# Optimization experiments

Hardware: AMD Instinct MI355X
Metric: run time of the kernel (lower is better)

## Reference

```python
import jax, jax.numpy as jnp
import numpy as np

T, B, F, H, N = 256, 256, 128, 1024, 2


def setup_inputs() -> dict:
    key = jax.random.key(0)
    ks = jax.random.split(key, 12)
    s_in = 1.0 / np.sqrt(H)  # PyTorch LSTM/Linear init scale ~ U(-1/sqrt(H), 1/sqrt(H))
    u = lambda k, shape: jax.random.uniform(k, shape, jnp.float32, -s_in, s_in)
    inp = {
        "x": jax.random.normal(ks[0], (T, B, F), jnp.float32),
        "W_ih0": u(ks[1], (4 * H, F)),
        "W_hh0": u(ks[2], (4 * H, H)),
        "b_ih0": u(ks[3], (4 * H,)),
        "b_hh0": u(ks[4], (4 * H,)),
        "W_ih1": u(ks[5], (4 * H, H)),
        "W_hh1": u(ks[6], (4 * H, H)),
        "b_ih1": u(ks[7], (4 * H,)),
        "b_hh1": u(ks[8], (4 * H,)),
        "W_lin": u(ks[9], (F, H)),
        "b_lin": u(ks[10], (F,)),
        "bs": B,
    }
    return inp


def _lstm_layer(x, W_ih, W_hh, b_ih, b_hh):
    # x: (T, B, in), returns out (T, B, H), (h_T, c_T) each (B, H)
    # Precompute input projections for all timesteps in one big GEMM.
    xW = jnp.einsum('tbf,gf->tbg', x, W_ih) + b_ih + b_hh  # (T, B, 4H)
    h0 = jnp.zeros((x.shape[1], W_hh.shape[1]), x.dtype)

    def step(carry, xw_t):
        h, c = carry
        gates = xw_t + h @ W_hh.T  # (B, 4H); PyTorch gate order i, f, g, o
        i, f, g, o = jnp.split(gates, 4, axis=-1)
        c = jax.nn.sigmoid(f) * c + jax.nn.sigmoid(i) * jnp.tanh(g)
        h = jax.nn.sigmoid(o) * jnp.tanh(c)
        return (h, c), h

    (h_T, c_T), out = jax.lax.scan(step, (h0, h0), xW)
    return out, h_T, c_T


def reference(x, W_ih0, W_hh0, b_ih0, b_hh0, W_ih1, W_hh1, b_ih1, b_hh1, W_lin, b_lin, bs):
    # Stacked 2-layer LSTM with zero initial state (self.h is None on fresh call).
    out0, h0_T, c0_T = _lstm_layer(x, W_ih0, W_hh0, b_ih0, b_hh0)
    out1, h1_T, c1_T = _lstm_layer(out0, W_ih1, W_hh1, b_ih1, b_hh1)
    # Original: y = linear(out[0]) -> first timestep of top layer output.
    y = out1[0] @ W_lin.T + b_lin  # (B, F)
    h_n = jnp.stack([h0_T, h1_T])  # (N, B, H)
    c_n = jnp.stack([c0_T, c1_T])  # (N, B, H)
    return y, h_n, c_n
```

## Files before the change

kernel.cpp:

```cpp
#include <hip/hip_runtime.h>
#include <stdint.h>


typedef __bf16 bf16x8 __attribute__((ext_vector_type(8)));
typedef float  f32x4  __attribute__((ext_vector_type(4)));
typedef unsigned short ushort8v __attribute__((ext_vector_type(8)));
typedef unsigned short ushort4v __attribute__((ext_vector_type(4)));
typedef unsigned short ushort2v __attribute__((ext_vector_type(2)));
typedef unsigned int   uint4v   __attribute__((ext_vector_type(4)));
typedef __attribute__((address_space(1))) unsigned int as1_u32;
typedef __attribute__((address_space(3))) unsigned int as3_u32;

#define T_STEPS 256
#define BATCH   256
#define HDIM    1024
#define GDIM    4096
#define FDIM    128
#define AS_STRIDE 2080

static __device__ __forceinline__ float bf2f(unsigned short u) {
  union { unsigned int i; float f; } v; v.i = ((unsigned int)u) << 16; return v.f;
}
static __device__ __forceinline__ unsigned short f2bf(float f) {
  return __builtin_bit_cast(unsigned short, (__bf16)f);
}
static __device__ __forceinline__ float sigm(float x) { return 1.f / (1.f + __expf(-x)); }
static __device__ __forceinline__ float tanh_f(float x) { return 2.f / (1.f + __expf(-2.f * x)) - 1.f; }

static __device__ __forceinline__ void vl1_inv() {
  asm volatile("buffer_inv" ::: "memory");
}

__global__ void conv_bf16(const float* __restrict__ s, unsigned short* __restrict__ d, int n) {
  int i = blockIdx.x * 256 + threadIdx.x;
  if (i < n) d[i] = f2bf(s[i]);
}

__global__ void diag_kernel(float* out, int n, float v) {
  int i = blockIdx.x * 256 + threadIdx.x;
  if (i < n) out[i] = v;
}

__device__ __forceinline__ void grp_arrive(unsigned int* gbar, bool fast) {
  __syncthreads();
  if (threadIdx.x == 0) {
    if (!fast) __builtin_amdgcn_fence(__ATOMIC_RELEASE, "agent");
    unsigned int my = __hip_atomic_fetch_add(&gbar[0], 1u, __ATOMIC_RELAXED, __HIP_MEMORY_SCOPE_AGENT);
    if ((my & 31u) == 31u)
      __hip_atomic_fetch_add(&gbar[32], 1u, __ATOMIC_RELAXED, __HIP_MEMORY_SCOPE_AGENT);
  }
}

__device__ __forceinline__ void grp_wait(unsigned int* gbar, unsigned int target, bool fast) {
  for (unsigned int it = 0; it < (1u << 14); ++it) {
    unsigned int g = __hip_atomic_load(&gbar[32], __ATOMIC_RELAXED, __HIP_MEMORY_SCOPE_AGENT);
    if ((int)(g - target) >= 0) break;
    __builtin_amdgcn_s_sleep(1);
  }
  if (!fast) __builtin_amdgcn_fence(__ATOMIC_ACQUIRE, "agent");
  else vl1_inv();
}

__device__ __forceinline__ void grp_barrier(unsigned int* gbar, unsigned int target, bool fast) {
  grp_arrive(gbar, fast);
  grp_wait(gbar, target, fast);
  __syncthreads();
}

__global__ __launch_bounds__(256) void gemm_bt_xw(
    const unsigned short* __restrict__ A,
    const unsigned short* __restrict__ B,
    unsigned short* __restrict__ xw,
    int K)
{
  const int tid = threadIdx.x, lane = tid & 63, w = tid >> 6;
  const int m0 = blockIdx.x * 128;
  const int n0 = blockIdx.y * 128;
  __shared__ unsigned short As[128 * 64];
  __shared__ unsigned short Bs[128 * 64];
  const int mrow0 = (w & 1) * 64, ncol0 = (w >> 1) * 64;
  const int quad = lane >> 4;

  f32x4 acc[4][4];
  #pragma unroll
  for (int i = 0; i < 4; ++i)
    #pragma unroll
    for (int j = 0; j < 4; ++j) acc[i][j] = f32x4{0.f, 0.f, 0.f, 0.f};

  const int kiter = K >> 6;
  for (int ki = 0; ki < kiter; ++ki) {
    const int k0 = ki * 64;
    __syncthreads();
    #pragma unroll
    for (int i = 0; i < 4; ++i) {
      int obase = (w * 4 + i) * 1024;
      int o = obase + lane * 16;
      int row = o >> 7; int kb = o & 127;
      const char* ga = (const char*)A + ((size_t)(m0 + row) * K + k0) * 2 + kb;
      const char* gb = (const char*)B + ((size_t)(n0 + row) * K + k0) * 2 + kb;
      __builtin_amdgcn_global_load_lds((const as1_u32*)ga, (as3_u32*)((char*)As + obase), 16, 0, 0);
      __builtin_amdgcn_global_load_lds((const as1_u32*)gb, (as3_u32*)((char*)Bs + obase), 16, 0, 0);
    }
    __syncthreads();
    #pragma unroll
    for (int kk = 0; kk < 2; ++kk) {
      bf16x8 af[4], bfr[4];
      #pragma unroll
      for (int mt = 0; mt < 4; ++mt)
        af[mt] = *(const bf16x8*)(As + (mrow0 + mt * 16 + (lane & 15)) * 64 + kk * 32 + quad * 8);
      #pragma unroll
      for (int nt = 0; nt < 4; ++nt)
        bfr[nt] = *(const bf16x8*)(Bs + (ncol0 + nt * 16 + (lane & 15)) * 64 + kk * 32 + quad * 8);
      #pragma unroll
      for (int mt = 0; mt < 4; ++mt)
        #pragma unroll
        for (int nt = 0; nt < 4; ++nt)
          acc[mt][nt] = __builtin_amdgcn_mfma_f32_16x16x32_bf16(af[mt], bfr[nt], acc[mt][nt], 0, 0, 0);
    }
  }
  #pragma unroll
  for (int mt = 0; mt < 4; ++mt) {
    int m = m0 + mrow0 + mt * 16 + quad * 4;
    int tl = m >> 8, b = m & 255;
    #pragma unroll
    for (int nt = 0; nt < 4; ++nt) {
      int col = n0 + ncol0 + nt * 16 + (lane & 15);
      ushort4v v;
      v.x = f2bf(acc[mt][nt][0]); v.y = f2bf(acc[mt][nt][1]);
      v.z = f2bf(acc[mt][nt][2]); v.w = f2bf(acc[mt][nt][3]);
      *(ushort4v*)(xw + ((size_t)tl * GDIM + col) * BATCH + b) = v;
    }
  }
}

__device__ __forceinline__ bool probe_fast(unsigned int* probe, unsigned int* gbar,
                                           unsigned int salt, unsigned int target,
                                           unsigned int* flagLds) {
  const int wg = blockIdx.x, mi = wg & 7;
  if (threadIdx.x == 0) probe[wg * 32] = salt ^ (unsigned int)wg;
  grp_barrier(gbar, target, true);
  if (threadIdx.x == 0) {
    unsigned int bad = 0;
    for (int k = 0; k < 32; ++k) {
      int member = mi + 8 * k;
      unsigned int v = probe[member * 32];
      if (v != (salt ^ (unsigned int)member)) bad = 1;
    }
    *flagLds = bad;
  }
  __syncthreads();
  return (*flagLds == 0);
}

__global__ __launch_bounds__(512, 2) void lstm_layer0_kernel(
    const unsigned short* __restrict__ xbf,
    const float* __restrict__ Wih,
    const float* __restrict__ Whh,
    const float* __restrict__ bih,
    const float* __restrict__ bhh,
    unsigned short* __restrict__ slab,
    float* __restrict__ cstate,
    int t0, int ch_len, unsigned int gen_base,
    float* __restrict__ dout_h,
    float* __restrict__ dout_c,
    unsigned int* __restrict__ bar,
    unsigned int* __restrict__ probe)
{
  const int tid = threadIdx.x, lane = tid & 63, wv = tid >> 6;
  const int quad = lane >> 4, l15 = lane & 15;
  const int g = wv & 3, kh = wv >> 2;
  const int wg = blockIdx.x;
  const int mi = wg & 7, ni = wg >> 3;
  const int r0 = mi * 32, hc0 = ni * 32;
  unsigned int* gbar = bar + mi * 64;

  __shared__ unsigned short As[32 * (AS_STRIDE / 2)];
  __shared__ float gbuf[8][32][36];
  __shared__ unsigned int flagLds;

  bf16x8 whh[2][16];
  #pragma unroll
  for (int nt = 0; nt < 2; ++nt) {
    const float* wrow = Whh + (size_t)(g * HDIM + hc0 + nt * 16 + l15) * HDIM + kh * 512 + quad * 8;
    #pragma unroll
    for (int kk = 0; kk < 16; ++kk) {
      f32x4 f0 = *(const f32x4*)(wrow + kk * 32);
      f32x4 f1 = *(const f32x4*)(wrow + kk * 32 + 4);
      bf16x8 r;
      r[0] = (__bf16)f0[0]; r[1] = (__bf16)f0[1]; r[2] = (__bf16)f0[2]; r[3] = (__bf16)f0[3];
      r[4] = (__bf16)f1[0]; r[5] = (__bf16)f1[1]; r[6] = (__bf16)f1[2]; r[7] = (__bf16)f1[3];
      whh[nt][kk] = r;
    }
  }
  bf16x8 wih[2][2];
  #pragma unroll
  for (int nt = 0; nt < 2; ++nt) {
    const float* wrow = Wih + (size_t)(g * HDIM + hc0 + nt * 16 + l15) * FDIM + kh * 64 + quad * 8;
    #pragma unroll
    for (int kk = 0; kk < 2; ++kk) {
      f32x4 f0 = *(const f32x4*)(wrow + kk * 32);
      f32x4 f1 = *(const f32x4*)(wrow + kk * 32 + 4);
      bf16x8 r;
      r[0] = (__bf16)f0[0]; r[1] = (__bf16)f0[1]; r[2] = (__bf16)f0[2]; r[3] = (__bf16)f0[3];
      r[4] = (__bf16)f1[0]; r[5] = (__bf16)f1[1]; r[6] = (__bf16)f1[2]; r[7] = (__bf16)f1[3];
      wih[nt][kk] = r;
    }
  }

  const int hcl = tid & 31, rg2 = tid >> 5;
  float bias[4];
  #pragma unroll
  for (int b4 = 0; b4 < 4; ++b4)
    bias[b4] = bih[b4 * HDIM + hc0 + hcl] + bhh[b4 * HDIM + hc0 + hcl];

  float c[2];
  #pragma unroll
  for (int r = 0; r < 2; ++r)
    c[r] = (t0 == 0) ? 0.f : cstate[(size_t)(r0 + rg2 * 2 + r) * HDIM + hc0 + hcl];

  unsigned int salt = 0x9E3779B9u ^ (gen_base * 2654435761u);
  bool fast = probe_fast(probe, gbar, salt, gen_base + 1u, &flagLds);

  const int tend = t0 + ch_len;

  f32x4 acc[2][2];
  #pragma unroll
  for (int mt = 0; mt < 2; ++mt)
    #pragma unroll
    for (int nt = 0; nt < 2; ++nt) acc[mt][nt] = f32x4{0.f, 0.f, 0.f, 0.f};
  #pragma unroll
  for (int j = 0; j < 2; ++j) {
    bf16x8 af[2];
    #pragma unroll
    for (int mt = 0; mt < 2; ++mt)
      af[mt] = *(const bf16x8*)(xbf + (size_t)(t0 * BATCH + r0 + mt * 16 + l15) * FDIM + kh * 64 + j * 32 + quad * 8);
    #pragma unroll
    for (int mt = 0; mt < 2; ++mt)
      #pragma unroll
      for (int nt = 0; nt < 2; ++nt)
        acc[mt][nt] = __builtin_amdgcn_mfma_f32_16x16x32_bf16(af[mt], wih[nt][j], acc[mt][nt], 0, 0, 0);
  }

  #pragma unroll 1
  for (int t = t0; t < tend; ++t) {
    if (t > 0) {
      const unsigned short* Aprev = slab + (size_t)(t - t0) * (BATCH * HDIM);
      #pragma unroll
      for (int p = 0; p < 8; ++p) {
        int idx = p * 8 + wv;
        int row = idx >> 1, half = idx & 1;
        const char* gsrc = (const char*)(Aprev + (size_t)(r0 + row) * HDIM + half * 512) + lane * 16;
        char* ldst = (char*)As + row * AS_STRIDE + half * 1024;
        __builtin_amdgcn_global_load_lds((const as1_u32*)gsrc, (as3_u32*)ldst, 16, 0, 0);
      }
      __syncthreads();
      #pragma unroll
      for (int j = 0; j < 16; ++j) {
        bf16x8 af[2];
        #pragma unroll
        for (int mt = 0; mt < 2; ++mt)
          af[mt] = *(const bf16x8*)((const char*)As + (mt * 16 + l15) * AS_STRIDE + (kh * 16 + j) * 64 + quad * 16);
        #pragma unroll
        for (int mt = 0; mt < 2; ++mt)
          #pragma unroll
          for (int nt = 0; nt < 2; ++nt)
            acc[mt][nt] = __builtin_amdgcn_mfma_f32_16x16x32_bf16(af[mt], whh[nt][j], acc[mt][nt], 0, 0, 0);
      }
    }

    __syncthreads();
    #pragma unroll
    for (int mt = 0; mt < 2; ++mt)
      #pragma unroll
      for (int nt = 0; nt < 2; ++nt) {
        int hl = nt * 16 + l15;
        int rq = mt * 16 + quad * 4;
        *(f32x4*)&gbuf[wv][hl][rq] = acc[mt][nt];
      }
    __syncthreads();

    unsigned short* hdst = slab + (size_t)(t - t0 + 1) * (BATCH * HDIM);
    unsigned short* hdst0 = slab;
    #pragma unroll
    for (int r = 0; r < 2; ++r) {
      int row = rg2 * 2 + r;
      float gi = gbuf[0][hcl][row] + gbuf[4][hcl][row] + bias[0];
      float gf = gbuf[1][hcl][row] + gbuf[5][hcl][row] + bias[1];
      float gg = gbuf[2][hcl][row] + gbuf[6][hcl][row] + bias[2];
      float go = gbuf[3][hcl][row] + gbuf[7][hcl][row] + bias[3];
      float iv = sigm(gi), fv = sigm(gf), gv = tanh_f(gg), ov = sigm(go);
      float cn = fv * c[r] + iv * gv;
      c[r] = cn;
      float hv = ov * tanh_f(cn);
      int gidx = (r0 + row) * HDIM + hc0 + hcl;
      unsigned short hb = f2bf(hv);
      hdst[gidx] = hb;
      if (t == tend - 1) { hdst0[gidx] = hb; cstate[gidx] = cn; }
      if (t == T_STEPS - 1) { dout_h[gidx] = hv; dout_c[gidx] = cn; }
    }

    if (t != tend - 1) {
      grp_arrive(gbar, fast);
      #pragma unroll
      for (int mt = 0; mt < 2; ++mt)
        #pragma unroll
        for (int nt = 0; nt < 2; ++nt) acc[mt][nt] = f32x4{0.f, 0.f, 0.f, 0.f};
      #pragma unroll
      for (int j = 0; j < 2; ++j) {
        bf16x8 af[2];
        #pragma unroll
        for (int mt = 0; mt < 2; ++mt)
          af[mt] = *(const bf16x8*)(xbf + (size_t)((t + 1) * BATCH + r0 + mt * 16 + l15) * FDIM + kh * 64 + j * 32 + quad * 8);
        #pragma unroll
        for (int mt = 0; mt < 2; ++mt)
          #pragma unroll
          for (int nt = 0; nt < 2; ++nt)
            acc[mt][nt] = __builtin_amdgcn_mfma_f32_16x16x32_bf16(af[mt], wih[nt][j], acc[mt][nt], 0, 0, 0);
      }
      grp_wait(gbar, gen_base + 2u + (unsigned int)(t - t0), fast);
    }
  }
}

__global__ __launch_bounds__(512, 2) void lstm_layer1_kernel(
    const unsigned short* __restrict__ xw,
    const float* __restrict__ Whh,
    const float* __restrict__ bih,
    const float* __restrict__ bhh,
    unsigned short* __restrict__ hpp,
    float* __restrict__ cstate,
    int t0, int ch_len, unsigned int gen_base,
    unsigned short* __restrict__ h1t0,
    float* __restrict__ dout_h,
    float* __restrict__ dout_c,
    unsigned int* __restrict__ bar,
    unsigned int* __restrict__ probe)
{
  const int tid = threadIdx.x, lane = tid & 63, wv = tid >> 6;
  const int quad = lane >> 4, l15 = lane & 15;
  const int g = wv & 3, kh = wv >> 2;
  const int wg = blockIdx.x;
  const int mi = wg & 7, ni = wg >> 3;
  const int r0 = mi * 32, hc0 = ni * 32;
  unsigned int* gbar = bar + mi * 64;

  __shared__ unsigned short As[32 * (AS_STRIDE / 2)];
  __shared__ float gbuf[8][32][36];
  __shared__ unsigned int flagLds;

  bf16x8 whh[2][16];
  #pragma unroll
  for (int nt = 0; nt < 2; ++nt) {
    const float* wrow = Whh + (size_t)(g * HDIM + hc0 + nt * 16 + l15) * HDIM + kh * 512 + quad * 8;
    #pragma unroll
    for (int kk = 0; kk < 16; ++kk) {
      f32x4 f0 = *(const f32x4*)(wrow + kk * 32);
      f32x4 f1 = *(const f32x4*)(wrow + kk * 32 + 4);
      bf16x8 r;
      r[0] = (__bf16)f0[0]; r[1] = (__bf16)f0[1]; r[2] = (__bf16)f0[2]; r[3] = (__bf16)f0[3];
      r[4] = (__bf16)f1[0]; r[5] = (__bf16)f1[1]; r[6] = (__bf16)f1[2]; r[7] = (__bf16)f1[3];
      whh[nt][kk] = r;
    }
  }

  const int hcl = tid & 31, rg2 = tid >> 5;
  float bias[4];
  #pragma unroll
  for (int b4 = 0; b4 < 4; ++b4)
    bias[b4] = bih[b4 * HDIM + hc0 + hcl] + bhh[b4 * HDIM + hc0 + hcl];

  float c[2];
  #pragma unroll
  for (int r = 0; r < 2; ++r)
    c[r] = (t0 == 0) ? 0.f : cstate[(size_t)(r0 + rg2 * 2 + r) * HDIM + hc0 + hcl];

  unsigned int salt = 0xB5297A4Du ^ (gen_base * 2654435761u);
  bool fast = probe_fast(probe, gbar, salt, gen_base + 1u, &flagLds);

  const int tend = t0 + ch_len;

  float xwv[4][2];
  #pragma unroll
  for (int g4 = 0; g4 < 4; ++g4) {
    const unsigned short* xp =
        xw + ((size_t)0 * GDIM + g4 * HDIM + hc0 + hcl) * BATCH + r0 + rg2 * 2;
    ushort2v u = *(const ushort2v*)xp;
    xwv[g4][0] = bf2f(u.x); xwv[g4][1] = bf2f(u.y);
  }

  #pragma unroll 1
  for (int t = t0; t < tend; ++t) {
    f32x4 acc[2][2];
    #pragma unroll
    for (int mt = 0; mt < 2; ++mt)
      #pragma unroll
      for (int nt = 0; nt < 2; ++nt) acc[mt][nt] = f32x4{0.f, 0.f, 0.f, 0.f};

    if (t > 0) {
      const unsigned short* Aprev = hpp + (size_t)((t - 1) & 1) * (BATCH * HDIM);
      #pragma unroll
      for (int p = 0; p < 8; ++p) {
        int idx = p * 8 + wv;
        int row = idx >> 1, half = idx & 1;
        const char* gsrc = (const char*)(Aprev + (size_t)(r0 + row) * HDIM + half * 512) + lane * 16;
        char* ldst = (char*)As + row * AS_STRIDE + half * 1024;
        __builtin_amdgcn_global_load_lds((const as1_u32*)gsrc, (as3_u32*)ldst, 16, 0, 0);
      }
      __syncthreads();
      #pragma unroll
      for (int j = 0; j < 16; ++j) {
        bf16x8 af[2];
        #pragma unroll
        for (int mt = 0; mt < 2; ++mt)
          af[mt] = *(const bf16x8*)((const char*)As + (mt * 16 + l15) * AS_STRIDE + (kh * 16 + j) * 64 + quad * 16);
        #pragma unroll
        for (int mt = 0; mt < 2; ++mt)
          #pragma unroll
          for (int nt = 0; nt < 2; ++nt)
            acc[mt][nt] = __builtin_amdgcn_mfma_f32_16x16x32_bf16(af[mt], whh[nt][j], acc[mt][nt], 0, 0, 0);
      }
    }

    __syncthreads();
    #pragma unroll
    for (int mt = 0; mt < 2; ++mt)
      #pragma unroll
      for (int nt = 0; nt < 2; ++nt) {
        int hl = nt * 16 + l15;
        int rq = mt * 16 + quad * 4;
        *(f32x4*)&gbuf[wv][hl][rq] = acc[mt][nt];
      }
    __syncthreads();

    unsigned short* hdst = hpp + (size_t)(t & 1) * (BATCH * HDIM);
    #pragma unroll
    for (int r = 0; r < 2; ++r) {
      int row = rg2 * 2 + r;
      float gi = gbuf[0][hcl][row] + gbuf[4][hcl][row] + xwv[0][r] + bias[0];
      float gf = gbuf[1][hcl][row] + gbuf[5][hcl][row] + xwv[1][r] + bias[1];
      float gg = gbuf[2][hcl][row] + gbuf[6][hcl][row] + xwv[2][r] + bias[2];
      float go = gbuf[3][hcl][row] + gbuf[7][hcl][row] + xwv[3][r] + bias[3];
      float iv = sigm(gi), fv = sigm(gf), gv = tanh_f(gg), ov = sigm(go);
      float cn = fv * c[r] + iv * gv;
      c[r] = cn;
      float hv = ov * tanh_f(cn);
      int gidx = (r0 + row) * HDIM + hc0 + hcl;
      hdst[gidx] = f2bf(hv);
      if (h1t0 != nullptr && t == 0) h1t0[gidx] = f2bf(hv);
      if (t == tend - 1) cstate[gidx] = cn;
      if (t == T_STEPS - 1) { dout_h[gidx] = hv; dout_c[gidx] = cn; }
    }

    if (t != tend - 1) {
      grp_arrive(gbar, fast);
      #pragma unroll
      for (int g4 = 0; g4 < 4; ++g4) {
        const unsigned short* xp =
            xw + ((size_t)(t + 1 - t0) * GDIM + g4 * HDIM + hc0 + hcl) * BATCH + r0 + rg2 * 2;
        ushort2v u = *(const ushort2v*)xp;
        xwv[g4][0] = bf2f(u.x); xwv[g4][1] = bf2f(u.y);
      }
      grp_wait(gbar, gen_base + 2u + (unsigned int)(t - t0), fast);
    }
  }
}

__global__ void y_kernel(const unsigned short* __restrict__ h1t0,
                         const unsigned short* __restrict__ wlin,
                         const float* __restrict__ blin,
                         float* __restrict__ y)
{
  int b = blockIdx.x;
  int f = threadIdx.x;
  const ushort8v* hp = (const ushort8v*)(h1t0 + (size_t)b * HDIM);
  const ushort8v* wp = (const ushort8v*)(wlin + (size_t)f * HDIM);
  float acc = 0.f;
  for (int i = 0; i < HDIM / 8; ++i) {
    ushort8v hv = hp[i], wvv = wp[i];
    #pragma unroll
    for (int j = 0; j < 8; ++j) acc += bf2f(hv[j]) * bf2f(wvv[j]);
  }
  y[b * FDIM + f] = acc + blin[f];
}

extern "C" void kernel_launch(void* const* d_in, const int* in_sizes, int n_in,
                              void* d_out, int out_size, void* d_ws, size_t ws_size,
                              hipStream_t stream) {
  (void)in_sizes; (void)n_in; (void)out_size;
  const float* x    = (const float*)d_in[0];
  const float* Wih0 = (const float*)d_in[1];
  const float* Whh0 = (const float*)d_in[2];
  const float* bih0 = (const float*)d_in[3];
  const float* bhh0 = (const float*)d_in[4];
  const float* Wih1 = (const float*)d_in[5];
  const float* Whh1 = (const float*)d_in[6];
  const float* bih1 = (const float*)d_in[7];
  const float* bhh1 = (const float*)d_in[8];
  const float* Wlin = (const float*)d_in[9];
  const float* blin = (const float*)d_in[10];
  float* out = (float*)d_out;

  const size_t SZ_BAR   = 4096;
  const size_t SZ_PROBE = 32768;
  const size_t SZ_XBF   = (size_t)T_STEPS * BATCH * FDIM * 2;
  const size_t SZ_WIH1  = (size_t)GDIM * HDIM * 2;
  const size_t SZ_WLIN  = (size_t)FDIM * HDIM * 2;
  const size_t SZ_HPP   = (size_t)2 * BATCH * HDIM * 2;
  const size_t SZ_H1T0  = (size_t)BATCH * HDIM * 2;
  const size_t SZ_CST   = (size_t)BATCH * HDIM * 4;
  const size_t SLOT     = (size_t)BATCH * HDIM * 2;
  const size_t fixed = SZ_BAR + SZ_PROBE + SZ_XBF + SZ_WIH1 + SZ_WLIN + SZ_HPP + SZ_H1T0 + 2 * SZ_CST;

  int CH = 0;
  const int cands[5] = {64, 32, 16, 8, 4};
  for (int i = 0; i < 5; ++i) {
    int c = cands[i];
    size_t need = fixed + (size_t)(c + 1) * SLOT + (size_t)c * GDIM * BATCH * 2;
    if (need <= ws_size) { CH = c; break; }
  }
  if (CH == 0) {
    float v = 1.0e6f + (float)(ws_size >> 20);
    diag_kernel<<<(32768 + 255) / 256, 256, 0, stream>>>(out, 32768, v);
    return;
  }

  char* ws = (char*)d_ws;
  size_t o = 0;
  unsigned int*   bar   = (unsigned int*)(ws + o);    o += SZ_BAR;
  unsigned int*   probe = (unsigned int*)(ws + o);    o += SZ_PROBE;
  unsigned short* xbf   = (unsigned short*)(ws + o);  o += SZ_XBF;
  unsigned short* wih1b = (unsigned short*)(ws + o);  o += SZ_WIH1;
  unsigned short* wlinb = (unsigned short*)(ws + o);  o += SZ_WLIN;
  unsigned short* h1pp  = (unsigned short*)(ws + o);  o += SZ_HPP;
  unsigned short* h1t0  = (unsigned short*)(ws + o);  o += SZ_H1T0;
  float*          c0st  = (float*)(ws + o);           o += SZ_CST;
  float*          c1st  = (float*)(ws + o);           o += SZ_CST;
  unsigned short* slab  = (unsigned short*)(ws + o);  o += (size_t)(CH + 1) * SLOT;
  unsigned short* xw1   = (unsigned short*)(ws + o);  o += (size_t)CH * GDIM * BATCH * 2;

  hipMemsetAsync(bar, 0, SZ_BAR, stream);

  conv_bf16<<<(T_STEPS * BATCH * FDIM + 255) / 256, 256, 0, stream>>>(x, xbf, T_STEPS * BATCH * FDIM);
  conv_bf16<<<(GDIM * HDIM + 255) / 256, 256, 0, stream>>>(Wih1, wih1b, GDIM * HDIM);
  conv_bf16<<<(FDIM * HDIM + 255) / 256, 256, 0, stream>>>(Wlin, wlinb, FDIM * HDIM);

  float* hn0 = out + 32768;
  float* hn1 = out + 32768 + 262144;
  float* cn0 = out + 32768 + 524288;
  float* cn1 = out + 32768 + 524288 + 262144;

  unsigned int gen_base = 0;
  for (int ch = 0; ch < T_STEPS / CH; ++ch) {
    int t0 = ch * CH;
    lstm_layer0_kernel<<<256, 512, 0, stream>>>(
        xbf, Wih0, Whh0, bih0, bhh0, slab, c0st, t0, CH, gen_base, hn0, cn0, bar, probe);
    gen_base += (unsigned int)CH;
    gemm_bt_xw<<<dim3(CH * 2, 32), 256, 0, stream>>>(
        slab + BATCH * HDIM, wih1b, xw1, HDIM);
    lstm_layer1_kernel<<<256, 512, 0, stream>>>(
        xw1, Whh1, bih1, bhh1, h1pp, c1st, t0, CH, gen_base, h1t0, hn1, cn1, bar, probe);
    gen_base += (unsigned int)CH;
  }

  y_kernel<<<256, 128, 0, stream>>>(h1t0, wlinb, blin, out);
}
```

Measured before the change: 3.631 ms.

## Split recurrent K dimension four ways with 1024-thread LSTM blocks

```diff
diff --git a/kernel.cpp b/kernel.cpp
--- a/kernel.cpp
+++ b/kernel.cpp
@@ -6,7 +6,6 @@
 typedef float  f32x4  __attribute__((ext_vector_type(4)));
 typedef unsigned short ushort8v __attribute__((ext_vector_type(8)));
 typedef unsigned short ushort4v __attribute__((ext_vector_type(4)));
-typedef unsigned short ushort2v __attribute__((ext_vector_type(2)));
 typedef unsigned int   uint4v   __attribute__((ext_vector_type(4)));
 typedef __attribute__((address_space(1))) unsigned int as1_u32;
 typedef __attribute__((address_space(3))) unsigned int as3_u32;
@@ -16,7 +15,7 @@
 #define HDIM    1024
 #define GDIM    4096
 #define FDIM    128
-#define AS_STRIDE 2080
+#define AS_STRIDE 2096
 
 static __device__ __forceinline__ float bf2f(unsigned short u) {
   union { unsigned int i; float f; } v; v.i = ((unsigned int)u) << 16; return v.f;
@@ -51,20 +50,22 @@
   }
 }
 
-__device__ __forceinline__ void grp_wait(unsigned int* gbar, unsigned int target, bool fast) {
-  for (unsigned int it = 0; it < (1u << 14); ++it) {
-    unsigned int g = __hip_atomic_load(&gbar[32], __ATOMIC_RELAXED, __HIP_MEMORY_SCOPE_AGENT);
-    if ((int)(g - target) >= 0) break;
-    __builtin_amdgcn_s_sleep(1);
-  }
-  if (!fast) __builtin_amdgcn_fence(__ATOMIC_ACQUIRE, "agent");
-  else vl1_inv();
-}
-
-__device__ __forceinline__ void grp_barrier(unsigned int* gbar, unsigned int target, bool fast) {
+__device__ __forceinline__ void grp_wait_w0(unsigned int* gbar, unsigned int target, bool fast, int wv) {
+  if (wv == 0) {
+    for (unsigned int it = 0; it < (1u << 14); ++it) {
+      unsigned int g = __hip_atomic_load(&gbar[32], __ATOMIC_RELAXED, __HIP_MEMORY_SCOPE_AGENT);
+      if ((int)(g - target) >= 0) break;
+      __builtin_amdgcn_s_sleep(1);
+    }
+    if (!fast) __builtin_amdgcn_fence(__ATOMIC_ACQUIRE, "agent");
+  }
+  __syncthreads();
+  if (fast) vl1_inv();
+}
+
+__device__ __forceinline__ void grp_barrier(unsigned int* gbar, unsigned int target, bool fast, int wv) {
   grp_arrive(gbar, fast);
-  grp_wait(gbar, target, fast);
-  __syncthreads();
+  grp_wait_w0(gbar, target, fast, wv);
 }
 
 __global__ __launch_bounds__(256) void gemm_bt_xw(
@@ -135,10 +136,10 @@
 
 __device__ __forceinline__ bool probe_fast(unsigned int* probe, unsigned int* gbar,
                                            unsigned int salt, unsigned int target,
-                                           unsigned int* flagLds) {
+                                           unsigned int* flagLds, int wv) {
   const int wg = blockIdx.x, mi = wg & 7;
   if (threadIdx.x == 0) probe[wg * 32] = salt ^ (unsigned int)wg;
-  grp_barrier(gbar, target, true);
+  grp_barrier(gbar, target, true, wv);
   if (threadIdx.x == 0) {
     unsigned int bad = 0;
     for (int k = 0; k < 32; ++k) {
@@ -152,13 +153,14 @@
   return (*flagLds == 0);
 }
 
-__global__ __launch_bounds__(512, 2) void lstm_layer0_kernel(
+__global__ __launch_bounds__(1024, 4) void lstm_layer0_kernel(
     const unsigned short* __restrict__ xbf,
     const float* __restrict__ Wih,
     const float* __restrict__ Whh,
     const float* __restrict__ bih,
     const float* __restrict__ bhh,
     unsigned short* __restrict__ slab,
+    unsigned short* __restrict__ hx,
     float* __restrict__ cstate,
     int t0, int ch_len, unsigned int gen_base,
     float* __restrict__ dout_h,
@@ -168,22 +170,22 @@
 {
   const int tid = threadIdx.x, lane = tid & 63, wv = tid >> 6;
   const int quad = lane >> 4, l15 = lane & 15;
-  const int g = wv & 3, kh = wv >> 2;
+  const int g = wv & 3, kq = wv >> 2;
   const int wg = blockIdx.x;
   const int mi = wg & 7, ni = wg >> 3;
   const int r0 = mi * 32, hc0 = ni * 32;
   unsigned int* gbar = bar + mi * 64;
 
   __shared__ unsigned short As[32 * (AS_STRIDE / 2)];
-  __shared__ float gbuf[8][32][36];
+  __shared__ float gbuf[16][32][33];
   __shared__ unsigned int flagLds;
 
-  bf16x8 whh[2][16];
+  bf16x8 whh[2][8];
   #pragma unroll
   for (int nt = 0; nt < 2; ++nt) {
-    const float* wrow = Whh + (size_t)(g * HDIM + hc0 + nt * 16 + l15) * HDIM + kh * 512 + quad * 8;
-    #pragma unroll
-    for (int kk = 0; kk < 16; ++kk) {
+    const float* wrow = Whh + (size_t)(g * HDIM + hc0 + nt * 16 + l15) * HDIM + kq * 256 + quad * 8;
+    #pragma unroll
+    for (int kk = 0; kk < 8; ++kk) {
       f32x4 f0 = *(const f32x4*)(wrow + kk * 32);
       f32x4 f1 = *(const f32x4*)(wrow + kk * 32 + 4);
       bf16x8 r;
@@ -192,34 +194,28 @@
       whh[nt][kk] = r;
     }
   }
-  bf16x8 wih[2][2];
+  bf16x8 wih[2];
   #pragma unroll
   for (int nt = 0; nt < 2; ++nt) {
-    const float* wrow = Wih + (size_t)(g * HDIM + hc0 + nt * 16 + l15) * FDIM + kh * 64 + quad * 8;
-    #pragma unroll
-    for (int kk = 0; kk < 2; ++kk) {
-      f32x4 f0 = *(const f32x4*)(wrow + kk * 32);
-      f32x4 f1 = *(const f32x4*)(wrow + kk * 32 + 4);
-      bf16x8 r;
-      r[0] = (__bf16)f0[0]; r[1] = (__bf16)f0[1]; r[2] = (__bf16)f0[2]; r[3] = (__bf16)f0[3];
-      r[4] = (__bf16)f1[0]; r[5] = (__bf16)f1[1]; r[6] = (__bf16)f1[2]; r[7] = (__bf16)f1[3];
-      wih[nt][kk] = r;
-    }
-  }
-
-  const int hcl = tid & 31, rg2 = tid >> 5;
+    const float* wrow = Wih + (size_t)(g * HDIM + hc0 + nt * 16 + l15) * FDIM + kq * 32 + quad * 8;
+    f32x4 f0 = *(const f32x4*)(wrow);
+    f32x4 f1 = *(const f32x4*)(wrow + 4);
+    bf16x8 r;
+    r[0] = (__bf16)f0[0]; r[1] = (__bf16)f0[1]; r[2] = (__bf16)f0[2]; r[3] = (__bf16)f0[3];
+    r[4] = (__bf16)f1[0]; r[5] = (__bf16)f1[1]; r[6] = (__bf16)f1[2]; r[7] = (__bf16)f1[3];
+    wih[nt] = r;
+  }
+
+  const int hcl = tid & 31, row = tid >> 5;
   float bias[4];
   #pragma unroll
   for (int b4 = 0; b4 < 4; ++b4)
     bias[b4] = bih[b4 * HDIM + hc0 + hcl] + bhh[b4 * HDIM + hc0 + hcl];
 
-  float c[2];
-  #pragma unroll
-  for (int r = 0; r < 2; ++r)
-    c[r] = (t0 == 0) ? 0.f : cstate[(size_t)(r0 + rg2 * 2 + r) * HDIM + hc0 + hcl];
+  float c1 = (t0 == 0) ? 0.f : cstate[(size_t)(r0 + row) * HDIM + hc0 + hcl];
 
   unsigned int salt = 0x9E3779B9u ^ (gen_base * 2654435761u);
-  bool fast = probe_fast(probe, gbar, salt, gen_base + 1u, &flagLds);
+  bool fast = probe_fast(probe, gbar, salt, gen_base + 1u, &flagLds, wv);
 
   const int tend = t0 + ch_len;
 
@@ -228,38 +224,37 @@
   for (int mt = 0; mt < 2; ++mt)
     #pragma unroll
     for (int nt = 0; nt < 2; ++nt) acc[mt][nt] = f32x4{0.f, 0.f, 0.f, 0.f};
-  #pragma unroll
-  for (int j = 0; j < 2; ++j) {
+  {
     bf16x8 af[2];
     #pragma unroll
     for (int mt = 0; mt < 2; ++mt)
-      af[mt] = *(const bf16x8*)(xbf + (size_t)(t0 * BATCH + r0 + mt * 16 + l15) * FDIM + kh * 64 + j * 32 + quad * 8);
+      af[mt] = *(const bf16x8*)(xbf + (size_t)(t0 * BATCH + r0 + mt * 16 + l15) * FDIM + kq * 32 + quad * 8);
     #pragma unroll
     for (int mt = 0; mt < 2; ++mt)
       #pragma unroll
       for (int nt = 0; nt < 2; ++nt)
-        acc[mt][nt] = __builtin_amdgcn_mfma_f32_16x16x32_bf16(af[mt], wih[nt][j], acc[mt][nt], 0, 0, 0);
+        acc[mt][nt] = __builtin_amdgcn_mfma_f32_16x16x32_bf16(af[mt], wih[nt], acc[mt][nt], 0, 0, 0);
   }
 
   #pragma unroll 1
   for (int t = t0; t < tend; ++t) {
     if (t > 0) {
-      const unsigned short* Aprev = slab + (size_t)(t - t0) * (BATCH * HDIM);
-      #pragma unroll
-      for (int p = 0; p < 8; ++p) {
-        int idx = p * 8 + wv;
-        int row = idx >> 1, half = idx & 1;
-        const char* gsrc = (const char*)(Aprev + (size_t)(r0 + row) * HDIM + half * 512) + lane * 16;
-        char* ldst = (char*)As + row * AS_STRIDE + half * 1024;
+      const unsigned short* Aprev = hx + (size_t)((t - 1) & 1) * (BATCH * HDIM);
+      #pragma unroll
+      for (int p = 0; p < 4; ++p) {
+        int idx = p * 16 + wv;
+        int arow = idx >> 1, half = idx & 1;
+        const char* gsrc = (const char*)(Aprev + (size_t)(r0 + arow) * HDIM + half * 512) + lane * 16;
+        char* ldst = (char*)As + arow * AS_STRIDE + half * 1024;
         __builtin_amdgcn_global_load_lds((const as1_u32*)gsrc, (as3_u32*)ldst, 16, 0, 0);
       }
       __syncthreads();
       #pragma unroll
-      for (int j = 0; j < 16; ++j) {
+      for (int j = 0; j < 8; ++j) {
         bf16x8 af[2];
         #pragma unroll
         for (int mt = 0; mt < 2; ++mt)
-          af[mt] = *(const bf16x8*)((const char*)As + (mt * 16 + l15) * AS_STRIDE + (kh * 16 + j) * 64 + quad * 16);
+          af[mt] = *(const bf16x8*)((const char*)As + (mt * 16 + l15) * AS_STRIDE + kq * 512 + j * 64 + quad * 16);
         #pragma unroll
         for (int mt = 0; mt < 2; ++mt)
           #pragma unroll
@@ -275,27 +270,28 @@
       for (int nt = 0; nt < 2; ++nt) {
         int hl = nt * 16 + l15;
         int rq = mt * 16 + quad * 4;
-        *(f32x4*)&gbuf[wv][hl][rq] = acc[mt][nt];
+        #pragma unroll
+        for (int i = 0; i < 4; ++i)
+          gbuf[wv][hl][rq + i] = acc[mt][nt][i];
       }
     __syncthreads();
 
     unsigned short* hdst = slab + (size_t)(t - t0 + 1) * (BATCH * HDIM);
-    unsigned short* hdst0 = slab;
-    #pragma unroll
-    for (int r = 0; r < 2; ++r) {
-      int row = rg2 * 2 + r;
-      float gi = gbuf[0][hcl][row] + gbuf[4][hcl][row] + bias[0];
-      float gf = gbuf[1][hcl][row] + gbuf[5][hcl][row] + bias[1];
-      float gg = gbuf[2][hcl][row] + gbuf[6][hcl][row] + bias[2];
-      float go = gbuf[3][hcl][row] + gbuf[7][hcl][row] + bias[3];
+    unsigned short* hxd  = hx + (size_t)(t & 1) * (BATCH * HDIM);
+    {
+      float gi = gbuf[0][hcl][row] + gbuf[4][hcl][row] + gbuf[8][hcl][row]  + gbuf[12][hcl][row] + bias[0];
+      float gf = gbuf[1][hcl][row] + gbuf[5][hcl][row] + gbuf[9][hcl][row]  + gbuf[13][hcl][row] + bias[1];
+      float gg = gbuf[2][hcl][row] + gbuf[6][hcl][row] + gbuf[10][hcl][row] + gbuf[14][hcl][row] + bias[2];
+      float go = gbuf[3][hcl][row] + gbuf[7][hcl][row] + gbuf[11][hcl][row] + gbuf[15][hcl][row] + bias[3];
       float iv = sigm(gi), fv = sigm(gf), gv = tanh_f(gg), ov = sigm(go);
-      float cn = fv * c[r] + iv * gv;
-      c[r] = cn;
+      float cn = fv * c1 + iv * gv;
+      c1 = cn;
       float hv = ov * tanh_f(cn);
       int gidx = (r0 + row) * HDIM + hc0 + hcl;
       unsigned short hb = f2bf(hv);
+      hxd[gidx] = hb;
       hdst[gidx] = hb;
-      if (t == tend - 1) { hdst0[gidx] = hb; cstate[gidx] = cn; }
+      if (t == tend - 1) cstate[gidx] = cn;
       if (t == T_STEPS - 1) { dout_h[gidx] = hv; dout_c[gidx] = cn; }
     }
 
@@ -305,24 +301,23 @@
       for (int mt = 0; mt < 2; ++mt)
         #pragma unroll
         for (int nt = 0; nt < 2; ++nt) acc[mt][nt] = f32x4{0.f, 0.f, 0.f, 0.f};
-      #pragma unroll
-      for (int j = 0; j < 2; ++j) {
+      {
         bf16x8 af[2];
         #pragma unroll
         for (int mt = 0; mt < 2; ++mt)
-          af[mt] = *(const bf16x8*)(xbf + (size_t)((t + 1) * BATCH + r0 + mt * 16 + l15) * FDIM + kh * 64 + j * 32 + quad * 8);
+          af[mt] = *(const bf16x8*)(xbf + (size_t)((t + 1) * BATCH + r0 + mt * 16 + l15) * FDIM + kq * 32 + quad * 8);
         #pragma unroll
         for (int mt = 0; mt < 2; ++mt)
           #pragma unroll
           for (int nt = 0; nt < 2; ++nt)
-            acc[mt][nt] = __builtin_amdgcn_mfma_f32_16x16x32_bf16(af[mt], wih[nt][j], acc[mt][nt], 0, 0, 0);
-      }
-      grp_wait(gbar, gen_base + 2u + (unsigned int)(t - t0), fast);
-    }
-  }
-}
-
-__global__ __launch_bounds__(512, 2) void lstm_layer1_kernel(
+            acc[mt][nt] = __builtin_amdgcn_mfma_f32_16x16x32_bf16(af[mt], wih[nt], acc[mt][nt], 0, 0, 0);
+      }
+      grp_wait_w0(gbar, gen_base + 2u + (unsigned int)(t - t0), fast, wv);
+    }
+  }
+}
+
+__global__ __launch_bounds__(1024, 4) void lstm_layer1_kernel(
     const unsigned short* __restrict__ xw,
     const float* __restrict__ Whh,
     const float* __restrict__ bih,
@@ -338,22 +333,22 @@
 {
   const int tid = threadIdx.x, lane = tid & 63, wv = tid >> 6;
   const int quad = lane >> 4, l15 = lane & 15;
-  const int g = wv & 3, kh = wv >> 2;
+  const int g = wv & 3, kq = wv >> 2;
   const int wg = blockIdx.x;
   const int mi = wg & 7, ni = wg >> 3;
   const int r0 = mi * 32, hc0 = ni * 32;
   unsigned int* gbar = bar + mi * 64;
 
   __shared__ unsigned short As[32 * (AS_STRIDE / 2)];
-  __shared__ float gbuf[8][32][36];
+  __shared__ float gbuf[16][32][33];
   __shared__ unsigned int flagLds;
 
-  bf16x8 whh[2][16];
+  bf16x8 whh[2][8];
   #pragma unroll
   for (int nt = 0; nt < 2; ++nt) {
-    const float* wrow = Whh + (size_t)(g * HDIM + hc0 + nt * 16 + l15) * HDIM + kh * 512 + quad * 8;
-    #pragma unroll
-    for (int kk = 0; kk < 16; ++kk) {
+    const float* wrow = Whh + (size_t)(g * HDIM + hc0 + nt * 16 + l15) * HDIM + kq * 256 + quad * 8;
+    #pragma unroll
+    for (int kk = 0; kk < 8; ++kk) {
       f32x4 f0 = *(const f32x4*)(wrow + kk * 32);
       f32x4 f1 = *(const f32x4*)(wrow + kk * 32 + 4);
       bf16x8 r;
@@ -363,29 +358,25 @@
     }
   }
 
-  const int hcl = tid & 31, rg2 = tid >> 5;
+  const int hcl = tid & 31, row = tid >> 5;
   float bias[4];
   #pragma unroll
   for (int b4 = 0; b4 < 4; ++b4)
     bias[b4] = bih[b4 * HDIM + hc0 + hcl] + bhh[b4 * HDIM + hc0 + hcl];
 
-  float c[2];
-  #pragma unroll
-  for (int r = 0; r < 2; ++r)
-    c[r] = (t0 == 0) ? 0.f : cstate[(size_t)(r0 + rg2 * 2 + r) * HDIM + hc0 + hcl];
+  float c1 = (t0 == 0) ? 0.f : cstate[(size_t)(r0 + row) * HDIM + hc0 + hcl];
 
   unsigned int salt = 0xB5297A4Du ^ (gen_base * 2654435761u);
-  bool fast = probe_fast(probe, gbar, salt, gen_base + 1u, &flagLds);
+  bool fast = probe_fast(probe, gbar, salt, gen_base + 1u, &flagLds, wv);
 
   const int tend = t0 + ch_len;
 
-  float xwv[4][2];
+  float xwv[4];
   #pragma unroll
   for (int g4 = 0; g4 < 4; ++g4) {
     const unsigned short* xp =
-        xw + ((size_t)0 * GDIM + g4 * HDIM + hc0 + hcl) * BATCH + r0 + rg2 * 2;
-    ushort2v u = *(const ushort2v*)xp;
-    xwv[g4][0] = bf2f(u.x); xwv[g4][1] = bf2f(u.y);
+        xw + ((size_t)0 * GDIM + g4 * HDIM + hc0 + hcl) * BATCH + r0 + row;
+    xwv[g4] = bf2f(*xp);
   }
 
   #pragma unroll 1
@@ -399,20 +390,20 @@
     if (t > 0) {
       const unsigned short* Aprev = hpp + (size_t)((t - 1) & 1) * (BATCH * HDIM);
       #pragma unroll
-      for (int p = 0; p < 8; ++p) {
-        int idx = p * 8 + wv;
-        int row = idx >> 1, half = idx & 1;
-        const char* gsrc = (const char*)(Aprev + (size_t)(r0 + row) * HDIM + half * 512) + lane * 16;
-        char* ldst = (char*)As + row * AS_STRIDE + half * 1024;
+      for (int p = 0; p < 4; ++p) {
+        int idx = p * 16 + wv;
+        int arow = idx >> 1, half = idx & 1;
+        const char* gsrc = (const char*)(Aprev + (size_t)(r0 + arow) * HDIM + half * 512) + lane * 16;
+        char* ldst = (char*)As + arow * AS_STRIDE + half * 1024;
         __builtin_amdgcn_global_load_lds((const as1_u32*)gsrc, (as3_u32*)ldst, 16, 0, 0);
       }
       __syncthreads();
       #pragma unroll
-      for (int j = 0; j < 16; ++j) {
+      for (int j = 0; j < 8; ++j) {
         bf16x8 af[2];
         #pragma unroll
         for (int mt = 0; mt < 2; ++mt)
-          af[mt] = *(const bf16x8*)((const char*)As + (mt * 16 + l15) * AS_STRIDE + (kh * 16 + j) * 64 + quad * 16);
+          af[mt] = *(const bf16x8*)((const char*)As + (mt * 16 + l15) * AS_STRIDE + kq * 512 + j * 64 + quad * 16);
         #pragma unroll
         for (int mt = 0; mt < 2; ++mt)
           #pragma unroll
@@ -428,21 +419,21 @@
       for (int nt = 0; nt < 2; ++nt) {
         int hl = nt * 16 + l15;
         int rq = mt * 16 + quad * 4;
-        *(f32x4*)&gbuf[wv][hl][rq] = acc[mt][nt];
+        #pragma unroll
+        for (int i = 0; i < 4; ++i)
+          gbuf[wv][hl][rq + i] = acc[mt][nt][i];
       }
     __syncthreads();
 
     unsigned short* hdst = hpp + (size_t)(t & 1) * (BATCH * HDIM);
-    #pragma unroll
-    for (int r = 0; r < 2; ++r) {
-      int row = rg2 * 2 + r;
-      float gi = gbuf[0][hcl][row] + gbuf[4][hcl][row] + xwv[0][r] + bias[0];
-      float gf = gbuf[1][hcl][row] + gbuf[5][hcl][row] + xwv[1][r] + bias[1];
-      float gg = gbuf[2][hcl][row] + gbuf[6][hcl][row] + xwv[2][r] + bias[2];
-      float go = gbuf[3][hcl][row] + gbuf[7][hcl][row] + xwv[3][r] + bias[3];
+    {
+      float gi = gbuf[0][hcl][row] + gbuf[4][hcl][row] + gbuf[8][hcl][row]  + gbuf[12][hcl][row] + xwv[0] + bias[0];
+      float gf = gbuf[1][hcl][row] + gbuf[5][hcl][row] + gbuf[9][hcl][row]  + gbuf[13][hcl][row] + xwv[1] + bias[1];
+      float gg = gbuf[2][hcl][row] + gbuf[6][hcl][row] + gbuf[10][hcl][row] + gbuf[14][hcl][row] + xwv[2] + bias[2];
+      float go = gbuf[3][hcl][row] + gbuf[7][hcl][row] + gbuf[11][hcl][row] + gbuf[15][hcl][row] + xwv[3] + bias[3];
       float iv = sigm(gi), fv = sigm(gf), gv = tanh_f(gg), ov = sigm(go);
-      float cn = fv * c[r] + iv * gv;
-      c[r] = cn;
+      float cn = fv * c1 + iv * gv;
+      c1 = cn;
       float hv = ov * tanh_f(cn);
       int gidx = (r0 + row) * HDIM + hc0 + hcl;
       hdst[gidx] = f2bf(hv);
@@ -456,11 +447,10 @@
       #pragma unroll
       for (int g4 = 0; g4 < 4; ++g4) {
         const unsigned short* xp =
-            xw + ((size_t)(t + 1 - t0) * GDIM + g4 * HDIM + hc0 + hcl) * BATCH + r0 + rg2 * 2;
-        ushort2v u = *(const ushort2v*)xp;
-        xwv[g4][0] = bf2f(u.x); xwv[g4][1] = bf2f(u.y);
-      }
-      grp_wait(gbar, gen_base + 2u + (unsigned int)(t - t0), fast);
+            xw + ((size_t)(t + 1 - t0) * GDIM + g4 * HDIM + hc0 + hcl) * BATCH + r0 + row;
+        xwv[g4] = bf2f(*xp);
+      }
+      grp_wait_w0(gbar, gen_base + 2u + (unsigned int)(t - t0), fast, wv);
     }
   }
 }
@@ -506,10 +496,11 @@
   const size_t SZ_WIH1  = (size_t)GDIM * HDIM * 2;
   const size_t SZ_WLIN  = (size_t)FDIM * HDIM * 2;
   const size_t SZ_HPP   = (size_t)2 * BATCH * HDIM * 2;
+  const size_t SZ_HX    = (size_t)2 * BATCH * HDIM * 2;
   const size_t SZ_H1T0  = (size_t)BATCH * HDIM * 2;
   const size_t SZ_CST   = (size_t)BATCH * HDIM * 4;
   const size_t SLOT     = (size_t)BATCH * HDIM * 2;
-  const size_t fixed = SZ_BAR + SZ_PROBE + SZ_XBF + SZ_WIH1 + SZ_WLIN + SZ_HPP + SZ_H1T0 + 2 * SZ_CST;
+  const size_t fixed = SZ_BAR + SZ_PROBE + SZ_XBF + SZ_WIH1 + SZ_WLIN + SZ_HPP + SZ_HX + SZ_H1T0 + 2 * SZ_CST;
 
   int CH = 0;
   const int cands[5] = {64, 32, 16, 8, 4};
@@ -532,6 +523,7 @@
   unsigned short* wih1b = (unsigned short*)(ws + o);  o += SZ_WIH1;
   unsigned short* wlinb = (unsigned short*)(ws + o);  o += SZ_WLIN;
   unsigned short* h1pp  = (unsigned short*)(ws + o);  o += SZ_HPP;
+  unsigned short* hx0   = (unsigned short*)(ws + o);  o += SZ_HX;
   unsigned short* h1t0  = (unsigned short*)(ws + o);  o += SZ_H1T0;
   float*          c0st  = (float*)(ws + o);           o += SZ_CST;
   float*          c1st  = (float*)(ws + o);           o += SZ_CST;
@@ -552,12 +544,12 @@
   unsigned int gen_base = 0;
   for (int ch = 0; ch < T_STEPS / CH; ++ch) {
     int t0 = ch * CH;
-    lstm_layer0_kernel<<<256, 512, 0, stream>>>(
-        xbf, Wih0, Whh0, bih0, bhh0, slab, c0st, t0, CH, gen_base, hn0, cn0, bar, probe);
+    lstm_layer0_kernel<<<256, 1024, 0, stream>>>(
+        xbf, Wih0, Whh0, bih0, bhh0, slab, hx0, c0st, t0, CH, gen_base, hn0, cn0, bar, probe);
     gen_base += (unsigned int)CH;
     gemm_bt_xw<<<dim3(CH * 2, 32), 256, 0, stream>>>(
         slab + BATCH * HDIM, wih1b, xw1, HDIM);
-    lstm_layer1_kernel<<<256, 512, 0, stream>>>(
+    lstm_layer1_kernel<<<256, 1024, 0, stream>>>(
         xw1, Whh1, bih1, bhh1, h1pp, c1st, t0, CH, gen_base, h1t0, hn1, cn1, bar, probe);
     gen_base += (unsigned int)CH;
   }
```

After: 3.956 ms. 9.0% more time.

## Replace counter barrier with per-block stamp polling and prefetch h into LDS

Applied to the files above, without the earlier changes.

```diff
diff --git a/kernel.cpp b/kernel.cpp
--- a/kernel.cpp
+++ b/kernel.cpp
@@ -41,30 +41,30 @@
   if (i < n) out[i] = v;
 }
 
-__device__ __forceinline__ void grp_arrive(unsigned int* gbar, bool fast) {
-  __syncthreads();
-  if (threadIdx.x == 0) {
-    if (!fast) __builtin_amdgcn_fence(__ATOMIC_RELEASE, "agent");
-    unsigned int my = __hip_atomic_fetch_add(&gbar[0], 1u, __ATOMIC_RELAXED, __HIP_MEMORY_SCOPE_AGENT);
-    if ((my & 31u) == 31u)
-      __hip_atomic_fetch_add(&gbar[32], 1u, __ATOMIC_RELAXED, __HIP_MEMORY_SCOPE_AGENT);
-  }
-}
-
-__device__ __forceinline__ void grp_wait(unsigned int* gbar, unsigned int target, bool fast) {
-  for (unsigned int it = 0; it < (1u << 14); ++it) {
-    unsigned int g = __hip_atomic_load(&gbar[32], __ATOMIC_RELAXED, __HIP_MEMORY_SCOPE_AGENT);
-    if ((int)(g - target) >= 0) break;
-    __builtin_amdgcn_s_sleep(1);
-  }
-  if (!fast) __builtin_amdgcn_fence(__ATOMIC_ACQUIRE, "agent");
-  else vl1_inv();
-}
-
-__device__ __forceinline__ void grp_barrier(unsigned int* gbar, unsigned int target, bool fast) {
-  grp_arrive(gbar, fast);
-  grp_wait(gbar, target, fast);
-  __syncthreads();
+__device__ __forceinline__ void post_stamp(unsigned int* st, unsigned int gen, bool fast) {
+  if (!fast) __builtin_amdgcn_fence(__ATOMIC_RELEASE, "agent");
+  __hip_atomic_store(st, gen, __ATOMIC_RELAXED, __HIP_MEMORY_SCOPE_AGENT);
+}
+
+__device__ __forceinline__ void poll_all(unsigned int* stamps, unsigned int target) {
+  unsigned int* p = stamps + (threadIdx.x & 31) * 32;
+  for (unsigned int it = 0; it < (1u << 15); ++it) {
+    unsigned int gv = __hip_atomic_load(p, __ATOMIC_RELAXED, __HIP_MEMORY_SCOPE_AGENT);
+    if (__all((int)(gv - target) >= 0)) return;
+    if (it > 16) __builtin_amdgcn_s_sleep(1);
+  }
+}
+
+__device__ __forceinline__ void stage64(const unsigned short* __restrict__ hsrc,
+                                        char* AsB, int r0, int wv, int lane) {
+  #pragma unroll
+  for (int p = 0; p < 8; ++p) {
+    int idx = p * 8 + wv;
+    int row = idx >> 1, half = idx & 1;
+    const char* gsrc = (const char*)(hsrc + (size_t)(r0 + row) * HDIM + half * 512) + lane * 16;
+    char* ldst = AsB + row * AS_STRIDE + half * 1024;
+    __builtin_amdgcn_global_load_lds((const as1_u32*)gsrc, (as3_u32*)ldst, 16, 0, 0);
+  }
 }
 
 __global__ __launch_bounds__(256) void gemm_bt_xw(
@@ -133,17 +133,22 @@
   }
 }
 
-__device__ __forceinline__ bool probe_fast(unsigned int* probe, unsigned int* gbar,
-                                           unsigned int salt, unsigned int target,
-                                           unsigned int* flagLds) {
-  const int wg = blockIdx.x, mi = wg & 7;
-  if (threadIdx.x == 0) probe[wg * 32] = salt ^ (unsigned int)wg;
-  grp_barrier(gbar, target, true);
-  if (threadIdx.x == 0) {
+__device__ __forceinline__ bool probe_chk(unsigned int* probeBuf, unsigned int* stamps,
+                                          unsigned int salt, unsigned int target,
+                                          unsigned int* flagLds) {
+  const int wg = blockIdx.x, mi = wg & 7, ni = wg >> 3;
+  const int tid = threadIdx.x;
+  if (tid == 0) probeBuf[wg * 32] = salt ^ (unsigned int)wg;
+  __syncthreads();
+  if (tid == 0)
+    __hip_atomic_store(stamps + ni * 32, target, __ATOMIC_RELAXED, __HIP_MEMORY_SCOPE_AGENT);
+  poll_all(stamps, target);
+  vl1_inv();
+  if (tid == 0) {
     unsigned int bad = 0;
     for (int k = 0; k < 32; ++k) {
       int member = mi + 8 * k;
-      unsigned int v = probe[member * 32];
+      unsigned int v = probeBuf[member * 32];
       if (v != (salt ^ (unsigned int)member)) bad = 1;
     }
     *flagLds = bad;
@@ -159,6 +164,7 @@
     const float* __restrict__ bih,
     const float* __restrict__ bhh,
     unsigned short* __restrict__ slab,
+    unsigned short* __restrict__ hx,
     float* __restrict__ cstate,
     int t0, int ch_len, unsigned int gen_base,
     float* __restrict__ dout_h,
@@ -172,7 +178,7 @@
   const int wg = blockIdx.x;
   const int mi = wg & 7, ni = wg >> 3;
   const int r0 = mi * 32, hc0 = ni * 32;
-  unsigned int* gbar = bar + mi * 64;
+  unsigned int* stamps = bar + mi * 1024;
 
   __shared__ unsigned short As[32 * (AS_STRIDE / 2)];
   __shared__ float gbuf[8][32][36];
@@ -219,9 +225,12 @@
     c[r] = (t0 == 0) ? 0.f : cstate[(size_t)(r0 + rg2 * 2 + r) * HDIM + hc0 + hcl];
 
   unsigned int salt = 0x9E3779B9u ^ (gen_base * 2654435761u);
-  bool fast = probe_fast(probe, gbar, salt, gen_base + 1u, &flagLds);
+  bool fast = probe_chk(probe, stamps, salt, gen_base + 1u, &flagLds);
 
   const int tend = t0 + ch_len;
+
+  if (t0 > 0)
+    stage64(hx + (size_t)((t0 - 1) & 1) * (BATCH * HDIM), (char*)As, r0, wv, lane);
 
   f32x4 acc[2][2];
   #pragma unroll
@@ -240,20 +249,11 @@
       for (int nt = 0; nt < 2; ++nt)
         acc[mt][nt] = __builtin_amdgcn_mfma_f32_16x16x32_bf16(af[mt], wih[nt][j], acc[mt][nt], 0, 0, 0);
   }
+  __syncthreads();
 
   #pragma unroll 1
   for (int t = t0; t < tend; ++t) {
     if (t > 0) {
-      const unsigned short* Aprev = slab + (size_t)(t - t0) * (BATCH * HDIM);
-      #pragma unroll
-      for (int p = 0; p < 8; ++p) {
-        int idx = p * 8 + wv;
-        int row = idx >> 1, half = idx & 1;
-        const char* gsrc = (const char*)(Aprev + (size_t)(r0 + row) * HDIM + half * 512) + lane * 16;
-        char* ldst = (char*)As + row * AS_STRIDE + half * 1024;
-        __builtin_amdgcn_global_load_lds((const as1_u32*)gsrc, (as3_u32*)ldst, 16, 0, 0);
-      }
-      __syncthreads();
       #pragma unroll
       for (int j = 0; j < 16; ++j) {
         bf16x8 af[2];
@@ -268,7 +268,6 @@
       }
     }
 
-    __syncthreads();
     #pragma unroll
     for (int mt = 0; mt < 2; ++mt)
       #pragma unroll
@@ -280,7 +279,7 @@
     __syncthreads();
 
     unsigned short* hdst = slab + (size_t)(t - t0 + 1) * (BATCH * HDIM);
-    unsigned short* hdst0 = slab;
+    unsigned short* hxd  = hx + (size_t)(t & 1) * (BATCH * HDIM);
     #pragma unroll
     for (int r = 0; r < 2; ++r) {
       int row = rg2 * 2 + r;
@@ -294,13 +293,17 @@
       float hv = ov * tanh_f(cn);
       int gidx = (r0 + row) * HDIM + hc0 + hcl;
       unsigned short hb = f2bf(hv);
+      hxd[gidx] = hb;
       hdst[gidx] = hb;
-      if (t == tend - 1) { hdst0[gidx] = hb; cstate[gidx] = cn; }
+      if (t == tend - 1) cstate[gidx] = cn;
       if (t == T_STEPS - 1) { dout_h[gidx] = hv; dout_c[gidx] = cn; }
     }
+    __syncthreads();
 
     if (t != tend - 1) {
-      grp_arrive(gbar, fast);
+      const unsigned int tgt = gen_base + 2u + (unsigned int)(t - t0);
+      if (tid == 0) post_stamp(stamps + ni * 32, tgt, fast);
+
       #pragma unroll
       for (int mt = 0; mt < 2; ++mt)
         #pragma unroll
@@ -317,7 +320,12 @@
           for (int nt = 0; nt < 2; ++nt)
             acc[mt][nt] = __builtin_amdgcn_mfma_f32_16x16x32_bf16(af[mt], wih[nt][j], acc[mt][nt], 0, 0, 0);
       }
-      grp_wait(gbar, gen_base + 2u + (unsigned int)(t - t0), fast);
+
+      poll_all(stamps, tgt);
+      if (fast) vl1_inv();
+      else __builtin_amdgcn_fence(__ATOMIC_ACQUIRE, "agent");
+      stage64(hx + (size_t)(t & 1) * (BATCH * HDIM), (char*)As, r0, wv, lane);
+      __syncthreads();
     }
   }
 }
@@ -342,7 +350,7 @@
   const int wg = blockIdx.x;
   const int mi = wg & 7, ni = wg >> 3;
   const int r0 = mi * 32, hc0 = ni * 32;
-  unsigned int* gbar = bar + mi * 64;
+  unsigned int* stamps = bar + mi * 1024;
 
   __shared__ unsigned short As[32 * (AS_STRIDE / 2)];
   __shared__ float gbuf[8][32][36];
@@ -375,10 +383,12 @@
     c[r] = (t0 == 0) ? 0.f : cstate[(size_t)(r0 + rg2 * 2 + r) * HDIM + hc0 + hcl];
 
   unsigned int salt = 0xB5297A4Du ^ (gen_base * 2654435761u);
-  bool fast = probe_fast(probe, gbar, salt, gen_base + 1u, &flagLds);
+  bool fast = probe_chk(probe, stamps, salt, gen_base + 1u, &flagLds);
 
   const int tend = t0 + ch_len;
 
+  if (t0 > 0)
+    stage64(hpp + (size_t)((t0 - 1) & 1) * (BATCH * HDIM), (char*)As, r0, wv, lane);
   float xwv[4][2];
   #pragma unroll
   for (int g4 = 0; g4 < 4; ++g4) {
@@ -387,6 +397,7 @@
     ushort2v u = *(const ushort2v*)xp;
     xwv[g4][0] = bf2f(u.x); xwv[g4][1] = bf2f(u.y);
   }
+  __syncthreads();
 
   #pragma unroll 1
   for (int t = t0; t < tend; ++t) {
@@ -397,16 +408,6 @@
       for (int nt = 0; nt < 2; ++nt) acc[mt][nt] = f32x4{0.f, 0.f, 0.f, 0.f};
 
     if (t > 0) {
-      const unsigned short* Aprev = hpp + (size_t)((t - 1) & 1) * (BATCH * HDIM);
-      #pragma unroll
-      for (int p = 0; p < 8; ++p) {
-        int idx = p * 8 + wv;
-        int row = idx >> 1, half = idx & 1;
-        const char* gsrc = (const char*)(Aprev + (size_t)(r0 + row) * HDIM + half * 512) + lane * 16;
-        char* ldst = (char*)As + row * AS_STRIDE + half * 1024;
-        __builtin_amdgcn_global_load_lds((const as1_u32*)gsrc, (as3_u32*)ldst, 16, 0, 0);
-      }
-      __syncthreads();
       #pragma unroll
       for (int j = 0; j < 16; ++j) {
         bf16x8 af[2];
@@ -421,7 +422,6 @@
       }
     }
 
-    __syncthreads();
     #pragma unroll
     for (int mt = 0; mt < 2; ++mt)
       #pragma unroll
@@ -450,9 +450,12 @@
       if (t == tend - 1) cstate[gidx] = cn;
       if (t == T_STEPS - 1) { dout_h[gidx] = hv; dout_c[gidx] = cn; }
     }
+    __syncthreads();
 
     if (t != tend - 1) {
-      grp_arrive(gbar, fast);
+      const unsigned int tgt = gen_base + 2u + (unsigned int)(t - t0);
+      if (tid == 0) post_stamp(stamps + ni * 32, tgt, fast);
+
       #pragma unroll
       for (int g4 = 0; g4 < 4; ++g4) {
         const unsigned short* xp =
@@ -460,7 +463,12 @@
         ushort2v u = *(const ushort2v*)xp;
         xwv[g4][0] = bf2f(u.x); xwv[g4][1] = bf2f(u.y);
       }
-      grp_wait(gbar, gen_base + 2u + (unsigned int)(t - t0), fast);
+
+      poll_all(stamps, tgt);
+      if (fast) vl1_inv();
+      else __builtin_amdgcn_fence(__ATOMIC_ACQUIRE, "agent");
+      stage64(hpp + (size_t)(t & 1) * (BATCH * HDIM), (char*)As, r0, wv, lane);
+      __syncthreads();
     }
   }
 }
@@ -500,16 +508,17 @@
   const float* blin = (const float*)d_in[10];
   float* out = (float*)d_out;
 
-  const size_t SZ_BAR   = 4096;
+  const size_t SZ_BAR   = 32768;
   const size_t SZ_PROBE = 32768;
   const size_t SZ_XBF   = (size_t)T_STEPS * BATCH * FDIM * 2;
   const size_t SZ_WIH1  = (size_t)GDIM * HDIM * 2;
   const size_t SZ_WLIN  = (size_t)FDIM * HDIM * 2;
   const size_t SZ_HPP   = (size_t)2 * BATCH * HDIM * 2;
+  const size_t SZ_HX    = (size_t)2 * BATCH * HDIM * 2;
   const size_t SZ_H1T0  = (size_t)BATCH * HDIM * 2;
   const size_t SZ_CST   = (size_t)BATCH * HDIM * 4;
   const size_t SLOT     = (size_t)BATCH * HDIM * 2;
-  const size_t fixed = SZ_BAR + SZ_PROBE + SZ_XBF + SZ_WIH1 + SZ_WLIN + SZ_HPP + SZ_H1T0 + 2 * SZ_CST;
+  const size_t fixed = SZ_BAR + SZ_PROBE + SZ_XBF + SZ_WIH1 + SZ_WLIN + SZ_HPP + SZ_HX + SZ_H1T0 + 2 * SZ_CST;
 
   int CH = 0;
   const int cands[5] = {64, 32, 16, 8, 4};
@@ -532,6 +541,7 @@
   unsigned short* wih1b = (unsigned short*)(ws + o);  o += SZ_WIH1;
   unsigned short* wlinb = (unsigned short*)(ws + o);  o += SZ_WLIN;
   unsigned short* h1pp  = (unsigned short*)(ws + o);  o += SZ_HPP;
+  unsigned short* hx0   = (unsigned short*)(ws + o);  o += SZ_HX;
   unsigned short* h1t0  = (unsigned short*)(ws + o);  o += SZ_H1T0;
   float*          c0st  = (float*)(ws + o);           o += SZ_CST;
   float*          c1st  = (float*)(ws + o);           o += SZ_CST;
@@ -553,7 +563,7 @@
   for (int ch = 0; ch < T_STEPS / CH; ++ch) {
     int t0 = ch * CH;
     lstm_layer0_kernel<<<256, 512, 0, stream>>>(
-        xbf, Wih0, Whh0, bih0, bhh0, slab, c0st, t0, CH, gen_base, hn0, cn0, bar, probe);
+        xbf, Wih0, Whh0, bih0, bhh0, slab, hx0, c0st, t0, CH, gen_base, hn0, cn0, bar, probe);
     gen_base += (unsigned int)CH;
     gemm_bt_xw<<<dim3(CH * 2, 32), 256, 0, stream>>>(
         slab + BATCH * HDIM, wih1b, xw1, HDIM);
```

Measured after the change: 3.610 ms. No clear change (-0.6%).
